# Performance work log

Hardware: AMD Instinct MI355X
Metric: run time of the kernel (lower is better)

## Reference

```python
import jax, jax.numpy as jnp
import numpy as np

N_NODES = 50000
N_EDGES = 800000
IN_FEATS = 128
HIDDEN = 256
N_CLASSES = 64


def setup_inputs() -> dict:
    key = jax.random.key(0)
    ks = jax.random.split(key, 16)
    def w(k, shape, fan_in):
        return jax.random.normal(k, shape, dtype=jnp.float32) * (1.0 / np.sqrt(fan_in))
    inp = {
        "x": jax.random.normal(ks[0], (N_NODES, IN_FEATS), dtype=jnp.float32),
        "edge_src": jax.random.randint(ks[1], (N_EDGES,), 0, N_NODES, dtype=jnp.int32),
        "edge_dst": jax.random.randint(ks[2], (N_EDGES,), 0, N_NODES, dtype=jnp.int32),
        # layer 0: in_feats -> hidden
        "W0s": w(ks[3], (IN_FEATS, HIDDEN), IN_FEATS),
        "W0n": w(ks[4], (IN_FEATS, HIDDEN), IN_FEATS),
        "b0": jnp.zeros((HIDDEN,), dtype=jnp.float32),
        # layer 1: hidden -> hidden
        "W1s": w(ks[5], (HIDDEN, HIDDEN), HIDDEN),
        "W1n": w(ks[6], (HIDDEN, HIDDEN), HIDDEN),
        "b1": jnp.zeros((HIDDEN,), dtype=jnp.float32),
        # layer 2: hidden -> hidden (last conv also outputs hidden per source code)
        "W2s": w(ks[7], (HIDDEN, HIDDEN), HIDDEN),
        "W2n": w(ks[8], (HIDDEN, HIDDEN), HIDDEN),
        "b2": jnp.zeros((HIDDEN,), dtype=jnp.float32),
        # fc1: hidden -> n_classes
        "Wfc": w(ks[9], (HIDDEN, N_CLASSES), HIDDEN),
        "bfc": jnp.zeros((N_CLASSES,), dtype=jnp.float32),
    }
    return inp


def _sage_layer(h, src, dst, Ws, Wn, b):
    # mean-neighbor aggregation: segment-sum messages, divide by in-degree
    msg = h[src]  # [E, D] irregular gather
    agg = jax.ops.segment_sum(msg, dst, num_segments=N_NODES)  # [N, D]
    deg = jax.ops.segment_sum(jnp.ones_like(dst, dtype=h.dtype), dst, num_segments=N_NODES)
    h_neigh = agg / jnp.maximum(deg, 1.0)[:, None]
    # DGL SAGEConv (mean): fc_self(h) + fc_neigh(h_neigh) + bias
    return h @ Ws + h_neigh @ Wn + b


def reference(x, edge_src, edge_dst, W0s, W0n, b0, W1s, W1n, b1, W2s, W2n, b2, Wfc, bfc):
    # forward applies dropout (identity at eval) and NO activation between layers,
    # matching the original module's forward().
    h = _sage_layer(x, edge_src, edge_dst, W0s, W0n, b0)
    h = _sage_layer(h, edge_src, edge_dst, W1s, W1n, b1)
    h = _sage_layer(h, edge_src, edge_dst, W2s, W2n, b2)
    return h @ Wfc + bfc  # [N, n_classes]
```

## Files before the change

kernel.cpp:

```cpp
#include <hip/hip_runtime.h>

#define NN 50000
#define NE 800000
#define NE_HALF 400000
#define F_IN 128
#define HID 256
#define N_CLS 64
#define SCAN_BLOCKS ((NN + 255) / 256)
#define HEPT 2
#define HBF ((NE + 256 * HEPT - 1) / (256 * HEPT))
#define HBH ((NE_HALF + 256 * HEPT - 1) / (256 * HEPT))
#define CF_BLOCKS 36
#define CL_BLOCKS 9
#define GA_BLOCKS ((NN + 127) / 128)
#define GG_BLOCKS ((NN + 31) / 32)
#define CROWS 515

typedef _Float16 half8 __attribute__((ext_vector_type(8)));
typedef float f32x4 __attribute__((ext_vector_type(4)));

__device__ __forceinline__ const float* virtC1_row(int r, const float* W0s,
                                                   const float* W0n, const float* b0) {
    if (r < 0) return nullptr;
    if (r < 128) return W0s + (size_t)r * 256;
    if (r < 256) return W0n + (size_t)(r - 128) * 256;
    if (r == 512) return b0;
    return nullptr;
}

__device__ __forceinline__ int shift_src(int r) {
    if (r >= 128 && r < 512) return r - 128;
    if (r == 513) return 512;
    if (r == 514) return 513;
    return -1;
}

__device__ __forceinline__ void compose_first_dev(
    int bx, const float* __restrict__ W0s, const float* __restrict__ W0n,
    const float* __restrict__ b0,
    const float* __restrict__ B1, const float* __restrict__ B2,
    const float* __restrict__ brow, float* __restrict__ C)
{
    __shared__ float As[64][17];
    __shared__ float Bs[16][64];
    const int tid = threadIdx.x;
    const int tx = tid & 15, ty = tid >> 4;
    const int row0 = (bx % 9) * 64;
    const int col0 = (bx / 9) * 64;
    const int lr = tid >> 2, lc = tid & 3;
    const int br = tid >> 4, bc = tid & 15;

    const int grow = row0 + lr;
    const int srcr0 = (grow < CROWS) ? grow : -1;
    const float* ap0 = virtC1_row(srcr0, W0s, W0n, b0);
    const float* ap1 = virtC1_row(shift_src(grow), W0s, W0n, b0);

    float acc[4][4] = {};

    float4 av = ap0 ? *(const float4*)(ap0 + lc * 4) : make_float4(0.f, 0.f, 0.f, 0.f);
    float4 bv = *(const float4*)(B1 + (size_t)br * 256 + col0 + bc * 4);

    for (int s = 0; s < 32; ++s) {
        As[lr][lc * 4 + 0] = av.x;
        As[lr][lc * 4 + 1] = av.y;
        As[lr][lc * 4 + 2] = av.z;
        As[lr][lc * 4 + 3] = av.w;
        *(float4*)&Bs[br][bc * 4] = bv;
        __syncthreads();
        if (s + 1 < 32) {
            int pass = (s + 1) >> 4;
            int k0 = ((s + 1) & 15) << 4;
            const float* ap = pass ? ap1 : ap0;
            const float* B = pass ? B2 : B1;
            av = ap ? *(const float4*)(ap + k0 + lc * 4) : make_float4(0.f, 0.f, 0.f, 0.f);
            bv = *(const float4*)(B + (size_t)(k0 + br) * 256 + col0 + bc * 4);
        }
        #pragma unroll
        for (int k = 0; k < 16; ++k) {
            float a[4];
            #pragma unroll
            for (int i = 0; i < 4; ++i) a[i] = As[ty * 4 + i][k];
            float4 bb = *(const float4*)&Bs[k][tx * 4];
            const float b[4] = {bb.x, bb.y, bb.z, bb.w};
            #pragma unroll
            for (int i = 0; i < 4; ++i)
                #pragma unroll
                for (int j = 0; j < 4; ++j)
                    acc[i][j] += a[i] * b[j];
        }
        __syncthreads();
    }

    #pragma unroll
    for (int i = 0; i < 4; ++i) {
        int r = row0 + ty * 4 + i;
        if (r < CROWS) {
            #pragma unroll
            for (int j = 0; j < 4; ++j) {
                float v = acc[i][j];
                if (r == 512) v += brow[col0 + tx * 4 + j];
                C[(size_t)r * 256 + col0 + tx * 4 + j] = v;
            }
        }
    }
}

__device__ __forceinline__ void compose_mid_dev(
    int bx, const float* __restrict__ A,
    const float* __restrict__ B1, const float* __restrict__ B2,
    const float* __restrict__ brow, float* __restrict__ C)
{
    __shared__ float As[64][17];
    __shared__ float Bs[16][64];
    const int tid = threadIdx.x;
    const int tx = tid & 15, ty = tid >> 4;
    const int row0 = (bx % 9) * 64;
    const int col0 = (bx / 9) * 64;
    const int lr = tid >> 2, lc = tid & 3;
    const int br = tid >> 4, bc = tid & 15;

    const int grow = row0 + lr;
    const int p0 = (grow < CROWS) ? grow : -1;
    const int p1 = shift_src(grow);

    float acc[4][4] = {};

    float4 av = (p0 >= 0) ? *(const float4*)(A + (size_t)p0 * 256 + lc * 4)
                          : make_float4(0.f, 0.f, 0.f, 0.f);
    float4 bv = *(const float4*)(B1 + (size_t)br * 256 + col0 + bc * 4);

    for (int s = 0; s < 32; ++s) {
        As[lr][lc * 4 + 0] = av.x;
        As[lr][lc * 4 + 1] = av.y;
        As[lr][lc * 4 + 2] = av.z;
        As[lr][lc * 4 + 3] = av.w;
        *(float4*)&Bs[br][bc * 4] = bv;
        __syncthreads();
        if (s + 1 < 32) {
            int pass = (s + 1) >> 4;
            int k0 = ((s + 1) & 15) << 4;
            int p = pass ? p1 : p0;
            const float* B = pass ? B2 : B1;
            av = (p >= 0) ? *(const float4*)(A + (size_t)p * 256 + k0 + lc * 4)
                          : make_float4(0.f, 0.f, 0.f, 0.f);
            bv = *(const float4*)(B + (size_t)(k0 + br) * 256 + col0 + bc * 4);
        }
        #pragma unroll
        for (int k = 0; k < 16; ++k) {
            float a[4];
            #pragma unroll
            for (int i = 0; i < 4; ++i) a[i] = As[ty * 4 + i][k];
            float4 bb = *(const float4*)&Bs[k][tx * 4];
            const float b[4] = {bb.x, bb.y, bb.z, bb.w};
            #pragma unroll
            for (int i = 0; i < 4; ++i)
                #pragma unroll
                for (int j = 0; j < 4; ++j)
                    acc[i][j] += a[i] * b[j];
        }
        __syncthreads();
    }

    #pragma unroll
    for (int i = 0; i < 4; ++i) {
        int r = row0 + ty * 4 + i;
        if (r < CROWS) {
            #pragma unroll
            for (int j = 0; j < 4; ++j) {
                float v = acc[i][j];
                if (r == 512) v += brow[col0 + tx * 4 + j];
                C[(size_t)r * 256 + col0 + tx * 4 + j] = v;
            }
        }
    }
}

__device__ __forceinline__ void compose_last_dev(
    int bx, const float* __restrict__ A, const float* __restrict__ B1,
    const float* __restrict__ brow, float* __restrict__ Vf, _Float16* __restrict__ BT)
{
    __shared__ float As[64][17];
    __shared__ float Bs[16][64];
    const int tid = threadIdx.x;
    const int tx = tid & 15, ty = tid >> 4;
    const int row0 = bx * 64;
    const int lr = tid >> 2, lc = tid & 3;
    const int br = tid >> 4, bc = tid & 15;

    const int grow = row0 + lr;
    const float* ap = (grow < CROWS) ? (A + (size_t)grow * 256) : nullptr;

    float acc[4][4] = {};

    float4 av = ap ? *(const float4*)(ap + lc * 4) : make_float4(0.f, 0.f, 0.f, 0.f);
    float4 bv = *(const float4*)(B1 + (size_t)br * 64 + bc * 4);

    for (int s = 0; s < 16; ++s) {
        As[lr][lc * 4 + 0] = av.x;
        As[lr][lc * 4 + 1] = av.y;
        As[lr][lc * 4 + 2] = av.z;
        As[lr][lc * 4 + 3] = av.w;
        *(float4*)&Bs[br][bc * 4] = bv;
        __syncthreads();
        if (s + 1 < 16) {
            int k0 = (s + 1) << 4;
            av = ap ? *(const float4*)(ap + k0 + lc * 4) : make_float4(0.f, 0.f, 0.f, 0.f);
            bv = *(const float4*)(B1 + (size_t)(k0 + br) * 64 + bc * 4);
        }
        #pragma unroll
        for (int k = 0; k < 16; ++k) {
            float a[4];
            #pragma unroll
            for (int i = 0; i < 4; ++i) a[i] = As[ty * 4 + i][k];
            float4 bb = *(const float4*)&Bs[k][tx * 4];
            const float b[4] = {bb.x, bb.y, bb.z, bb.w};
            #pragma unroll
            for (int i = 0; i < 4; ++i)
                #pragma unroll
                for (int j = 0; j < 4; ++j)
                    acc[i][j] += a[i] * b[j];
        }
        __syncthreads();
    }

    #pragma unroll
    for (int i = 0; i < 4; ++i) {
        int r = row0 + ty * 4 + i;
        if (r < CROWS) {
            #pragma unroll
            for (int j = 0; j < 4; ++j) {
                int c = tx * 4 + j;
                float v = acc[i][j];
                if (r == 512) v += brow[c];
                Vf[(size_t)r * 64 + c] = v;
                if (r < 512)
                    BT[(size_t)((r >> 7) * 64 + c) * 128 + (r & 127)] = (_Float16)v;
            }
        }
    }
}

__device__ __forceinline__ void hist_dev(int bx, int start, int count,
                                         const int* __restrict__ edst,
                                         int* __restrict__ cnt,
                                         unsigned short* __restrict__ rank) {
    int base = start + bx * (256 * HEPT) + threadIdx.x;
    int lim = start + count;
    int d[HEPT];
    #pragma unroll
    for (int k = 0; k < HEPT; ++k) {
        int e = base + k * 256;
        d[k] = (e < lim) ? edst[e] : -1;
    }
    #pragma unroll
    for (int k = 0; k < HEPT; ++k) {
        int e = base + k * 256;
        if (d[k] >= 0) rank[e] = (unsigned short)atomicAdd(&cnt[d[k]], 1);
    }
}

__device__ __forceinline__ void scan_full_dev(const int* __restrict__ cnt,
                                              int* __restrict__ offs,
                                              float* __restrict__ dinv, int bx) {
    __shared__ int s[256];
    const int t = threadIdx.x;
    const int limit = bx * 256;
    int p = 0;
    for (int i = t; i < limit; i += 256) p += cnt[i];
    s[t] = p;
    __syncthreads();
    for (int off = 128; off > 0; off >>= 1) {
        if (t < off) s[t] += s[t + off];
        __syncthreads();
    }
    const int base = s[0];
    __syncthreads();
    int i = limit + t;
    int v = (i < NN) ? cnt[i] : 0;
    s[t] = v;
    __syncthreads();
    for (int off = 1; off < 256; off <<= 1) {
        int u = (t >= off) ? s[t - off] : 0;
        __syncthreads();
        s[t] += u;
        __syncthreads();
    }
    if (i < NN) {
        offs[i] = base + s[t] - v;
        dinv[i] = 1.0f / (float)max(v, 1);
    }
    if (i == NN - 1) offs[NN] = base + s[t];
}

__device__ __forceinline__ void gemm_y_dev(
    int bx, int by,
    const float* __restrict__ X, const _Float16* __restrict__ BT,
    _Float16* __restrict__ Y, _Float16* __restrict__ Tc, int N)
{
    constexpr int LP = 40;
    __shared__ _Float16 As[128 * LP];
    __shared__ _Float16 Bs[128 * LP];

    const int tid = threadIdx.x;
    const int wave = tid >> 6;
    const int lane = tid & 63;
    const int l15 = lane & 15;
    const int quad = lane >> 4;
    const int wrow = wave >> 1;
    const int wcol = wave & 1;
    const int m_base = wrow * 64;
    const int n_base = wcol * 64;

    const int row0 = bx * 128;
    const int col0 = by * 128;

    f32x4 acc[4][4] = {};

    for (int k0 = 0; k0 < 128; k0 += 32) {
        #pragma unroll
        for (int r = 0; r < 2; ++r) {
            int idx = r * 256 + tid;
            int row = idx >> 2, ch = idx & 3;
            int gr = row0 + row; if (gr > N - 1) gr = N - 1;
            const float* ap = X + (size_t)gr * 128 + k0 + ch * 8;
            float4 f0 = *(const float4*)ap;
            float4 f1 = *(const float4*)(ap + 4);
            half8 v = { (_Float16)f0.x, (_Float16)f0.y, (_Float16)f0.z, (_Float16)f0.w,
                        (_Float16)f1.x, (_Float16)f1.y, (_Float16)f1.z, (_Float16)f1.w };
            *(half8*)&As[row * LP + ch * 8] = v;
        }
        #pragma unroll
        for (int r = 0; r < 2; ++r) {
            int idx = r * 256 + tid;
            int row = idx >> 2, ch = idx & 3;
            *(half8*)&Bs[row * LP + ch * 8] =
                *(const half8*)(BT + (size_t)(col0 + row) * 128 + k0 + ch * 8);
        }
        __syncthreads();
        half8 af[4], bf[4];
        #pragma unroll
        for (int i = 0; i < 4; ++i)
            af[i] = *(const half8*)&As[(m_base + i * 16 + l15) * LP + quad * 8];
        #pragma unroll
        for (int j = 0; j < 4; ++j)
            bf[j] = *(const half8*)&Bs[(n_base + j * 16 + l15) * LP + quad * 8];
        #pragma unroll
        for (int i = 0; i < 4; ++i)
            #pragma unroll
            for (int j = 0; j < 4; ++j)
                acc[i][j] = __builtin_amdgcn_mfma_f32_16x16x32_f16(af[i], bf[j], acc[i][j], 0, 0, 0);
        __syncthreads();
    }

    #pragma unroll
    for (int i = 0; i < 4; ++i) {
        #pragma unroll
        for (int j = 0; j < 4; ++j) {
            int col = col0 + n_base + j * 16 + l15;
            #pragma unroll
            for (int r = 0; r < 4; ++r) {
                int row = row0 + m_base + i * 16 + quad * 4 + r;
                if (row < N) {
                    _Float16 v = (_Float16)acc[i][j][r];
                    Y[(size_t)row * 256 + col] = v;
                    if (col >= 192) Tc[(size_t)row * 64 + (col - 192)] = v;
                }
            }
        }
    }
}

template <bool OUT_F32>
__device__ __forceinline__ void gather_node_dev(
    int node, int lane,
    const _Float16* __restrict__ Tin,
    const unsigned short* __restrict__ csr, const int* __restrict__ offs,
    const float* __restrict__ dinv,
    const _Float16* __restrict__ Yadd,
    const float* __restrict__ cvec,
    void* __restrict__ Tout)
{
    int beg = offs[node], end = offs[node + 1];
    float acc[8] = {};
    int e = beg;
    for (; e + 7 < end; e += 8) {
        int s0 = csr[e], s1 = csr[e + 1], s2 = csr[e + 2], s3 = csr[e + 3];
        int s4 = csr[e + 4], s5 = csr[e + 5], s6 = csr[e + 6], s7 = csr[e + 7];
        half8 v0 = *(const half8*)(Tin + (size_t)s0 * 64 + lane * 8);
        half8 v1 = *(const half8*)(Tin + (size_t)s1 * 64 + lane * 8);
        half8 v2 = *(const half8*)(Tin + (size_t)s2 * 64 + lane * 8);
        half8 v3 = *(const half8*)(Tin + (size_t)s3 * 64 + lane * 8);
        half8 v4 = *(const half8*)(Tin + (size_t)s4 * 64 + lane * 8);
        half8 v5 = *(const half8*)(Tin + (size_t)s5 * 64 + lane * 8);
        half8 v6 = *(const half8*)(Tin + (size_t)s6 * 64 + lane * 8);
        half8 v7 = *(const half8*)(Tin + (size_t)s7 * 64 + lane * 8);
        #pragma unroll
        for (int j = 0; j < 8; ++j)
            acc[j] += (((float)v0[j] + (float)v1[j]) + ((float)v2[j] + (float)v3[j]))
                    + (((float)v4[j] + (float)v5[j]) + ((float)v6[j] + (float)v7[j]));
    }
    for (; e + 3 < end; e += 4) {
        int s0 = csr[e], s1 = csr[e + 1], s2 = csr[e + 2], s3 = csr[e + 3];
        half8 v0 = *(const half8*)(Tin + (size_t)s0 * 64 + lane * 8);
        half8 v1 = *(const half8*)(Tin + (size_t)s1 * 64 + lane * 8);
        half8 v2 = *(const half8*)(Tin + (size_t)s2 * 64 + lane * 8);
        half8 v3 = *(const half8*)(Tin + (size_t)s3 * 64 + lane * 8);
        #pragma unroll
        for (int j = 0; j < 8; ++j)
            acc[j] += ((float)v0[j] + (float)v1[j]) + ((float)v2[j] + (float)v3[j]);
    }
    for (; e < end; ++e) {
        half8 v = *(const half8*)(Tin + (size_t)csr[e] * 64 + lane * 8);
        #pragma unroll
        for (int j = 0; j < 8; ++j) acc[j] += (float)v[j];
    }
    float sc = dinv[node];
    half8 y = *(const half8*)(Yadd + (size_t)node * 256 + lane * 8);
    if (OUT_F32) {
        float* o = (float*)Tout + (size_t)node * 64 + lane * 8;
        float4 o0, o1;
        o0.x = acc[0] * sc + (float)y[0] + cvec[lane * 8 + 0];
        o0.y = acc[1] * sc + (float)y[1] + cvec[lane * 8 + 1];
        o0.z = acc[2] * sc + (float)y[2] + cvec[lane * 8 + 2];
        o0.w = acc[3] * sc + (float)y[3] + cvec[lane * 8 + 3];
        o1.x = acc[4] * sc + (float)y[4] + cvec[lane * 8 + 4];
        o1.y = acc[5] * sc + (float)y[5] + cvec[lane * 8 + 5];
        o1.z = acc[6] * sc + (float)y[6] + cvec[lane * 8 + 6];
        o1.w = acc[7] * sc + (float)y[7] + cvec[lane * 8 + 7];
        *(float4*)o = o0;
        *(float4*)(o + 4) = o1;
    } else {
        half8 o;
        #pragma unroll
        for (int j = 0; j < 8; ++j)
            o[j] = (_Float16)(acc[j] * sc + (float)y[j] + cvec[lane * 8 + j]);
        *(half8*)((_Float16*)Tout + (size_t)node * 64 + lane * 8) = o;
    }
}

__global__ __launch_bounds__(256) void k_composeF_hist(
    const int* __restrict__ edst, int* __restrict__ cnt, unsigned short* __restrict__ rank,
    const float* __restrict__ W0s, const float* __restrict__ W0n, const float* __restrict__ b0,
    const float* __restrict__ W1s, const float* __restrict__ W1n, const float* __restrict__ b1,
    float* __restrict__ C2)
{
    if (blockIdx.x < CF_BLOCKS) {
        compose_first_dev(blockIdx.x, W0s, W0n, b0, W1s, W1n, b1, C2);
    } else {
        hist_dev(blockIdx.x - CF_BLOCKS, 0, NE_HALF, edst, cnt, rank);
    }
}

__global__ __launch_bounds__(256) void k_composeM_hist2(
    const int* __restrict__ edst, int* __restrict__ cnt, unsigned short* __restrict__ rank,
    const float* __restrict__ C2,
    const float* __restrict__ W2s, const float* __restrict__ W2n, const float* __restrict__ b2,
    float* __restrict__ C3)
{
    if (blockIdx.x < CF_BLOCKS) compose_mid_dev(blockIdx.x, C2, W2s, W2n, b2, C3);
    else hist_dev(blockIdx.x - CF_BLOCKS, NE_HALF, NE - NE_HALF, edst, cnt, rank);
}

__global__ __launch_bounds__(256) void k_composeL_scan(
    const int* __restrict__ cnt, int* __restrict__ offs, float* __restrict__ dinv,
    const float* __restrict__ C3, const float* __restrict__ Wfc, const float* __restrict__ bfc,
    float* __restrict__ Vf, _Float16* __restrict__ BT)
{
    if (blockIdx.x < CL_BLOCKS) compose_last_dev(blockIdx.x, C3, Wfc, bfc, Vf, BT);
    else scan_full_dev(cnt, offs, dinv, blockIdx.x - CL_BLOCKS);
}

__global__ __launch_bounds__(256) void k_gemmT_place(
    const int* __restrict__ esrc, const int* __restrict__ edst,
    const unsigned short* __restrict__ rank, const int* __restrict__ offs,
    unsigned short* __restrict__ csr,
    const float* __restrict__ X, const _Float16* __restrict__ BT,
    _Float16* __restrict__ Y, _Float16* __restrict__ Tc)
{
    if (blockIdx.x < GA_BLOCKS) {
        gemm_y_dev(blockIdx.x, 1, X, BT, Y, Tc, NN);
    } else {
        int base = (blockIdx.x - GA_BLOCKS) * (256 * HEPT) + threadIdx.x;
        int d[HEPT], s[HEPT], r[HEPT];
        #pragma unroll
        for (int k = 0; k < HEPT; ++k) {
            int e = base + k * 256;
            if (e < NE) { d[k] = edst[e]; s[k] = esrc[e]; r[k] = rank[e]; }
            else d[k] = -1;
        }
        #pragma unroll
        for (int k = 0; k < HEPT; ++k) {
            if (d[k] >= 0) csr[offs[d[k]] + r[k]] = (unsigned short)s[k];
        }
    }
}

__global__ __launch_bounds__(256) void k_gemmA_gather1(
    const float* __restrict__ X, const _Float16* __restrict__ BT,
    _Float16* __restrict__ Y, _Float16* __restrict__ Tc,
    const unsigned short* __restrict__ csr, const int* __restrict__ offs,
    const float* __restrict__ dinv, const float* __restrict__ Vf,
    _Float16* __restrict__ Ta)
{
    if (blockIdx.x < GA_BLOCKS) {
        gemm_y_dev(blockIdx.x, 0, X, BT, Y, Tc, NN);
    } else {
        int node = (blockIdx.x - GA_BLOCKS) * 32 + (threadIdx.x >> 3);
        int lane = threadIdx.x & 7;
        if (node < NN)
            gather_node_dev<false>(node, lane, Tc, csr, offs, dinv,
                                   Y + 128, Vf + (size_t)514 * 64, (void*)Ta);
    }
}

template <bool OUT_F32>
__global__ __launch_bounds__(256) void gather64(
    const _Float16* __restrict__ Tin,
    const unsigned short* __restrict__ csr, const int* __restrict__ offs,
    const float* __restrict__ dinv,
    const _Float16* __restrict__ Yadd,
    const float* __restrict__ cvec,
    void* __restrict__ Tout, int N)
{
    int node = blockIdx.x * 32 + (threadIdx.x >> 3);
    int lane = threadIdx.x & 7;
    if (node >= N) return;
    gather_node_dev<OUT_F32>(node, lane, Tin, csr, offs, dinv, Yadd, cvec, Tout);
}

extern "C" void kernel_launch(void* const* d_in, const int* in_sizes, int n_in,
                              void* d_out, int out_size, void* d_ws, size_t ws_size,
                              hipStream_t stream) {
    const float* x    = (const float*)d_in[0];
    const int*   esrc = (const int*)d_in[1];
    const int*   edst = (const int*)d_in[2];
    const float* W0s  = (const float*)d_in[3];
    const float* W0n  = (const float*)d_in[4];
    const float* b0   = (const float*)d_in[5];
    const float* W1s  = (const float*)d_in[6];
    const float* W1n  = (const float*)d_in[7];
    const float* b1   = (const float*)d_in[8];
    const float* W2s  = (const float*)d_in[9];
    const float* W2n  = (const float*)d_in[10];
    const float* b2   = (const float*)d_in[11];
    const float* Wfc  = (const float*)d_in[12];
    const float* bfc  = (const float*)d_in[13];
    float* out = (float*)d_out;

    _Float16* Y   = (_Float16*)d_ws;
    _Float16* Ta  = Y + (size_t)NN * 256;
    _Float16* Tb  = Ta + (size_t)NN * 64;
    _Float16* Tc  = Tb + (size_t)NN * 64;
    _Float16* BT  = Tc + (size_t)NN * 64;
    float* C2     = (float*)(BT + 256 * 128);
    float* C3     = C2 + CROWS * 256;
    float* Vf     = C3 + CROWS * 256;
    float* dinv   = Vf + CROWS * 64;
    int* cnt      = (int*)(dinv + NN);
    int* offs     = cnt + NN;
    int* blockSums = offs + NN + 1;
    unsigned short* rank = (unsigned short*)(blockSums + SCAN_BLOCKS);
    unsigned short* csr  = rank + NE;

    hipMemsetAsync(cnt, 0, (size_t)NN * sizeof(int), stream);

    k_composeF_hist<<<CF_BLOCKS + HBH, 256, 0, stream>>>(
        edst, cnt, rank, W0s, W0n, b0, W1s, W1n, b1, C2);

    k_composeM_hist2<<<CF_BLOCKS + HBH, 256, 0, stream>>>(
        edst, cnt, rank, C2, W2s, W2n, b2, C3);

    k_composeL_scan<<<CL_BLOCKS + SCAN_BLOCKS, 256, 0, stream>>>(
        cnt, offs, dinv, C3, Wfc, bfc, Vf, BT);

    k_gemmT_place<<<GA_BLOCKS + HBF, 256, 0, stream>>>(
        esrc, edst, rank, offs, csr, x, BT, Y, Tc);

    k_gemmA_gather1<<<GA_BLOCKS + GG_BLOCKS, 256, 0, stream>>>(
        x, BT, Y, Tc, csr, offs, dinv, Vf, Ta);

    gather64<false><<<GG_BLOCKS, 256, 0, stream>>>(
        Ta, csr, offs, dinv, Y + 64, Vf + (size_t)513 * 64, (void*)Tb, NN);
    gather64<true><<<GG_BLOCKS, 256, 0, stream>>>(
        Tb, csr, offs, dinv, Y, Vf + (size_t)512 * 64, (void*)out, NN);
}
```

Measured before the change: 284.4 us.

## Reassociate weight composition and merge launches into fewer fused kernels

The weight-chain composition is reassociated: W2s·Wfc and W2n·Wfc (plus the combined bias) are precomputed in parallel with the first composition and the edge histogram. The separate mid and last compose stages become a single 515x64 compose. This removes one full 515x256x512 GEMM stage and one kernel launch. The whole histogram now runs in one kernel with 4 edges per thread. Both node GEMM passes run together with CSR placement. The first gather becomes its own launch, so it no longer overlaps with a GEMM.

```diff
diff --git a/kernel.cpp b/kernel.cpp
--- a/kernel.cpp
+++ b/kernel.cpp
@@ -2,16 +2,15 @@
 
 #define NN 50000
 #define NE 800000
-#define NE_HALF 400000
 #define F_IN 128
 #define HID 256
 #define N_CLS 64
 #define SCAN_BLOCKS ((NN + 255) / 256)
-#define HEPT 2
+#define HEPT 4
 #define HBF ((NE + 256 * HEPT - 1) / (256 * HEPT))
-#define HBH ((NE_HALF + 256 * HEPT - 1) / (256 * HEPT))
 #define CF_BLOCKS 36
-#define CL_BLOCKS 9
+#define PRE_BLOCKS 9
+#define CFIN_BLOCKS 9
 #define GA_BLOCKS ((NN + 127) / 128)
 #define GG_BLOCKS ((NN + 31) / 32)
 #define CROWS 515
@@ -105,45 +104,44 @@
     }
 }
 
-__device__ __forceinline__ void compose_mid_dev(
-    int bx, const float* __restrict__ A,
-    const float* __restrict__ B1, const float* __restrict__ B2,
-    const float* __restrict__ brow, float* __restrict__ C)
-{
+__device__ __forceinline__ void precompute_dev(
+    int p, const float* __restrict__ W2s, const float* __restrict__ W2n,
+    const float* __restrict__ b2, const float* __restrict__ Wfc, const float* __restrict__ bfc,
+    float* __restrict__ Wcs, float* __restrict__ Wcn, float* __restrict__ bcv)
+{
+    const int tid = threadIdx.x;
+    if (p == 8) {
+        if (tid < 64) {
+            float s = bfc[tid];
+            for (int k = 0; k < 256; ++k) s += b2[k] * Wfc[(size_t)k * 64 + tid];
+            bcv[tid] = s;
+        }
+        return;
+    }
     __shared__ float As[64][17];
     __shared__ float Bs[16][64];
-    const int tid = threadIdx.x;
     const int tx = tid & 15, ty = tid >> 4;
-    const int row0 = (bx % 9) * 64;
-    const int col0 = (bx / 9) * 64;
     const int lr = tid >> 2, lc = tid & 3;
     const int br = tid >> 4, bc = tid & 15;
-
-    const int grow = row0 + lr;
-    const int p0 = (grow < CROWS) ? grow : -1;
-    const int p1 = shift_src(grow);
+    const float* M = (p < 4) ? W2s : W2n;
+    float* O = (p < 4) ? Wcs : Wcn;
+    const int row0 = (p & 3) * 64;
 
     float acc[4][4] = {};
-
-    float4 av = (p0 >= 0) ? *(const float4*)(A + (size_t)p0 * 256 + lc * 4)
-                          : make_float4(0.f, 0.f, 0.f, 0.f);
-    float4 bv = *(const float4*)(B1 + (size_t)br * 256 + col0 + bc * 4);
-
-    for (int s = 0; s < 32; ++s) {
+    float4 av = *(const float4*)(M + (size_t)(row0 + lr) * 256 + lc * 4);
+    float4 bv = *(const float4*)(Wfc + (size_t)br * 64 + bc * 4);
+
+    for (int s = 0; s < 16; ++s) {
         As[lr][lc * 4 + 0] = av.x;
         As[lr][lc * 4 + 1] = av.y;
         As[lr][lc * 4 + 2] = av.z;
         As[lr][lc * 4 + 3] = av.w;
         *(float4*)&Bs[br][bc * 4] = bv;
         __syncthreads();
-        if (s + 1 < 32) {
-            int pass = (s + 1) >> 4;
-            int k0 = ((s + 1) & 15) << 4;
-            int p = pass ? p1 : p0;
-            const float* B = pass ? B2 : B1;
-            av = (p >= 0) ? *(const float4*)(A + (size_t)p * 256 + k0 + lc * 4)
-                          : make_float4(0.f, 0.f, 0.f, 0.f);
-            bv = *(const float4*)(B + (size_t)(k0 + br) * 256 + col0 + bc * 4);
+        if (s + 1 < 16) {
+            int k0 = (s + 1) << 4;
+            av = *(const float4*)(M + (size_t)(row0 + lr) * 256 + k0 + lc * 4);
+            bv = *(const float4*)(Wfc + (size_t)(k0 + br) * 64 + bc * 4);
         }
         #pragma unroll
         for (int k = 0; k < 16; ++k) {
@@ -160,24 +158,18 @@
         }
         __syncthreads();
     }
-
     #pragma unroll
-    for (int i = 0; i < 4; ++i) {
-        int r = row0 + ty * 4 + i;
-        if (r < CROWS) {
-            #pragma unroll
-            for (int j = 0; j < 4; ++j) {
-                float v = acc[i][j];
-                if (r == 512) v += brow[col0 + tx * 4 + j];
-                C[(size_t)r * 256 + col0 + tx * 4 + j] = v;
-            }
-        }
-    }
-}
-
-__device__ __forceinline__ void compose_last_dev(
-    int bx, const float* __restrict__ A, const float* __restrict__ B1,
-    const float* __restrict__ brow, float* __restrict__ Vf, _Float16* __restrict__ BT)
+    for (int i = 0; i < 4; ++i)
+        #pragma unroll
+        for (int j = 0; j < 4; ++j)
+            O[(size_t)(row0 + ty * 4 + i) * 64 + tx * 4 + j] = acc[i][j];
+}
+
+__device__ __forceinline__ void compose_fin_dev(
+    int bx, const float* __restrict__ C2,
+    const float* __restrict__ Wcs, const float* __restrict__ Wcn,
+    const float* __restrict__ bcv,
+    float* __restrict__ Vf, _Float16* __restrict__ BT)
 {
     __shared__ float As[64][17];
     __shared__ float Bs[16][64];
@@ -188,24 +180,30 @@
     const int br = tid >> 4, bc = tid & 15;
 
     const int grow = row0 + lr;
-    const float* ap = (grow < CROWS) ? (A + (size_t)grow * 256) : nullptr;
+    const int p0 = (grow < CROWS) ? grow : -1;
+    const int p1 = shift_src(grow);
 
     float acc[4][4] = {};
 
-    float4 av = ap ? *(const float4*)(ap + lc * 4) : make_float4(0.f, 0.f, 0.f, 0.f);
-    float4 bv = *(const float4*)(B1 + (size_t)br * 64 + bc * 4);
-
-    for (int s = 0; s < 16; ++s) {
+    float4 av = (p0 >= 0) ? *(const float4*)(C2 + (size_t)p0 * 256 + lc * 4)
+                          : make_float4(0.f, 0.f, 0.f, 0.f);
+    float4 bv = *(const float4*)(Wcs + (size_t)br * 64 + bc * 4);
+
+    for (int s = 0; s < 32; ++s) {
         As[lr][lc * 4 + 0] = av.x;
         As[lr][lc * 4 + 1] = av.y;
         As[lr][lc * 4 + 2] = av.z;
         As[lr][lc * 4 + 3] = av.w;
         *(float4*)&Bs[br][bc * 4] = bv;
         __syncthreads();
-        if (s + 1 < 16) {
-            int k0 = (s + 1) << 4;
-            av = ap ? *(const float4*)(ap + k0 + lc * 4) : make_float4(0.f, 0.f, 0.f, 0.f);
-            bv = *(const float4*)(B1 + (size_t)(k0 + br) * 64 + bc * 4);
+        if (s + 1 < 32) {
+            int pass = (s + 1) >> 4;
+            int k0 = ((s + 1) & 15) << 4;
+            int p = pass ? p1 : p0;
+            const float* B = pass ? Wcn : Wcs;
+            av = (p >= 0) ? *(const float4*)(C2 + (size_t)p * 256 + k0 + lc * 4)
+                          : make_float4(0.f, 0.f, 0.f, 0.f);
+            bv = *(const float4*)(B + (size_t)(k0 + br) * 64 + bc * 4);
         }
         #pragma unroll
         for (int k = 0; k < 16; ++k) {
@@ -231,7 +229,7 @@
             for (int j = 0; j < 4; ++j) {
                 int c = tx * 4 + j;
                 float v = acc[i][j];
-                if (r == 512) v += brow[c];
+                if (r == 512) v += bcv[c];
                 Vf[(size_t)r * 64 + c] = v;
                 if (r < 512)
                     BT[(size_t)((r >> 7) * 64 + c) * 128 + (r & 127)] = (_Float16)v;
@@ -240,17 +238,15 @@
     }
 }
 
-__device__ __forceinline__ void hist_dev(int bx, int start, int count,
-                                         const int* __restrict__ edst,
+__device__ __forceinline__ void hist_dev(int bx, const int* __restrict__ edst,
                                          int* __restrict__ cnt,
                                          unsigned short* __restrict__ rank) {
-    int base = start + bx * (256 * HEPT) + threadIdx.x;
-    int lim = start + count;
+    int base = bx * (256 * HEPT) + threadIdx.x;
     int d[HEPT];
     #pragma unroll
     for (int k = 0; k < HEPT; ++k) {
         int e = base + k * 256;
-        d[k] = (e < lim) ? edst[e] : -1;
+        d[k] = (e < NE) ? edst[e] : -1;
     }
     #pragma unroll
     for (int k = 0; k < HEPT; ++k) {
@@ -438,39 +434,35 @@
     }
 }
 
-__global__ __launch_bounds__(256) void k_composeF_hist(
+__global__ __launch_bounds__(256) void k_CF_pre_hist(
     const int* __restrict__ edst, int* __restrict__ cnt, unsigned short* __restrict__ rank,
     const float* __restrict__ W0s, const float* __restrict__ W0n, const float* __restrict__ b0,
     const float* __restrict__ W1s, const float* __restrict__ W1n, const float* __restrict__ b1,
-    float* __restrict__ C2)
+    const float* __restrict__ W2s, const float* __restrict__ W2n, const float* __restrict__ b2,
+    const float* __restrict__ Wfc, const float* __restrict__ bfc,
+    float* __restrict__ C2, float* __restrict__ Wcs, float* __restrict__ Wcn,
+    float* __restrict__ bcv)
 {
     if (blockIdx.x < CF_BLOCKS) {
         compose_first_dev(blockIdx.x, W0s, W0n, b0, W1s, W1n, b1, C2);
+    } else if (blockIdx.x < CF_BLOCKS + PRE_BLOCKS) {
+        precompute_dev(blockIdx.x - CF_BLOCKS, W2s, W2n, b2, Wfc, bfc, Wcs, Wcn, bcv);
     } else {
-        hist_dev(blockIdx.x - CF_BLOCKS, 0, NE_HALF, edst, cnt, rank);
-    }
-}
-
-__global__ __launch_bounds__(256) void k_composeM_hist2(
-    const int* __restrict__ edst, int* __restrict__ cnt, unsigned short* __restrict__ rank,
-    const float* __restrict__ C2,
-    const float* __restrict__ W2s, const float* __restrict__ W2n, const float* __restrict__ b2,
-    float* __restrict__ C3)
-{
-    if (blockIdx.x < CF_BLOCKS) compose_mid_dev(blockIdx.x, C2, W2s, W2n, b2, C3);
-    else hist_dev(blockIdx.x - CF_BLOCKS, NE_HALF, NE - NE_HALF, edst, cnt, rank);
-}
-
-__global__ __launch_bounds__(256) void k_composeL_scan(
+        hist_dev(blockIdx.x - CF_BLOCKS - PRE_BLOCKS, edst, cnt, rank);
+    }
+}
+
+__global__ __launch_bounds__(256) void k_CFin_scan(
     const int* __restrict__ cnt, int* __restrict__ offs, float* __restrict__ dinv,
-    const float* __restrict__ C3, const float* __restrict__ Wfc, const float* __restrict__ bfc,
+    const float* __restrict__ C2, const float* __restrict__ Wcs,
+    const float* __restrict__ Wcn, const float* __restrict__ bcv,
     float* __restrict__ Vf, _Float16* __restrict__ BT)
 {
-    if (blockIdx.x < CL_BLOCKS) compose_last_dev(blockIdx.x, C3, Wfc, bfc, Vf, BT);
-    else scan_full_dev(cnt, offs, dinv, blockIdx.x - CL_BLOCKS);
-}
-
-__global__ __launch_bounds__(256) void k_gemmT_place(
+    if (blockIdx.x < CFIN_BLOCKS) compose_fin_dev(blockIdx.x, C2, Wcs, Wcn, bcv, Vf, BT);
+    else scan_full_dev(cnt, offs, dinv, blockIdx.x - CFIN_BLOCKS);
+}
+
+__global__ __launch_bounds__(256) void k_gemm_place(
     const int* __restrict__ esrc, const int* __restrict__ edst,
     const unsigned short* __restrict__ rank, const int* __restrict__ offs,
     unsigned short* __restrict__ csr,
@@ -479,8 +471,10 @@
 {
     if (blockIdx.x < GA_BLOCKS) {
         gemm_y_dev(blockIdx.x, 1, X, BT, Y, Tc, NN);
+    } else if (blockIdx.x < 2 * GA_BLOCKS) {
+        gemm_y_dev(blockIdx.x - GA_BLOCKS, 0, X, BT, Y, Tc, NN);
     } else {
-        int base = (blockIdx.x - GA_BLOCKS) * (256 * HEPT) + threadIdx.x;
+        int base = (blockIdx.x - 2 * GA_BLOCKS) * (256 * HEPT) + threadIdx.x;
         int d[HEPT], s[HEPT], r[HEPT];
         #pragma unroll
         for (int k = 0; k < HEPT; ++k) {
@@ -492,24 +486,6 @@
         for (int k = 0; k < HEPT; ++k) {
             if (d[k] >= 0) csr[offs[d[k]] + r[k]] = (unsigned short)s[k];
         }
-    }
-}
-
-__global__ __launch_bounds__(256) void k_gemmA_gather1(
-    const float* __restrict__ X, const _Float16* __restrict__ BT,
-    _Float16* __restrict__ Y, _Float16* __restrict__ Tc,
-    const unsigned short* __restrict__ csr, const int* __restrict__ offs,
-    const float* __restrict__ dinv, const float* __restrict__ Vf,
-    _Float16* __restrict__ Ta)
-{
-    if (blockIdx.x < GA_BLOCKS) {
-        gemm_y_dev(blockIdx.x, 0, X, BT, Y, Tc, NN);
-    } else {
-        int node = (blockIdx.x - GA_BLOCKS) * 32 + (threadIdx.x >> 3);
-        int lane = threadIdx.x & 7;
-        if (node < NN)
-            gather_node_dev<false>(node, lane, Tc, csr, offs, dinv,
-                                   Y + 128, Vf + (size_t)514 * 64, (void*)Ta);
     }
 }
 
@@ -553,32 +529,30 @@
     _Float16* Tc  = Tb + (size_t)NN * 64;
     _Float16* BT  = Tc + (size_t)NN * 64;
     float* C2     = (float*)(BT + 256 * 128);
-    float* C3     = C2 + CROWS * 256;
-    float* Vf     = C3 + CROWS * 256;
+    float* Wcs    = C2 + CROWS * 256;
+    float* Wcn    = Wcs + 256 * 64;
+    float* bcv    = Wcn + 256 * 64;
+    float* Vf     = bcv + 64;
     float* dinv   = Vf + CROWS * 64;
     int* cnt      = (int*)(dinv + NN);
     int* offs     = cnt + NN;
-    int* blockSums = offs + NN + 1;
-    unsigned short* rank = (unsigned short*)(blockSums + SCAN_BLOCKS);
+    unsigned short* rank = (unsigned short*)(offs + NN + 1);
     unsigned short* csr  = rank + NE;
 
     hipMemsetAsync(cnt, 0, (size_t)NN * sizeof(int), stream);
 
-    k_composeF_hist<<<CF_BLOCKS + HBH, 256, 0, stream>>>(
-        edst, cnt, rank, W0s, W0n, b0, W1s, W1n, b1, C2);
-
-    k_composeM_hist2<<<CF_BLOCKS + HBH, 256, 0, stream>>>(
-        edst, cnt, rank, C2, W2s, W2n, b2, C3);
-
-    k_composeL_scan<<<CL_BLOCKS + SCAN_BLOCKS, 256, 0, stream>>>(
-        cnt, offs, dinv, C3, Wfc, bfc, Vf, BT);
-
-    k_gemmT_place<<<GA_BLOCKS + HBF, 256, 0, stream>>>(
+    k_CF_pre_hist<<<CF_BLOCKS + PRE_BLOCKS + HBF, 256, 0, stream>>>(
+        edst, cnt, rank, W0s, W0n, b0, W1s, W1n, b1,
+        W2s, W2n, b2, Wfc, bfc, C2, Wcs, Wcn, bcv);
+
+    k_CFin_scan<<<CFIN_BLOCKS + SCAN_BLOCKS, 256, 0, stream>>>(
+        cnt, offs, dinv, C2, Wcs, Wcn, bcv, Vf, BT);
+
+    k_gemm_place<<<2 * GA_BLOCKS + HBF, 256, 0, stream>>>(
         esrc, edst, rank, offs, csr, x, BT, Y, Tc);
 
-    k_gemmA_gather1<<<GA_BLOCKS + GG_BLOCKS, 256, 0, stream>>>(
-        x, BT, Y, Tc, csr, offs, dinv, Vf, Ta);
-
+    gather64<false><<<GG_BLOCKS, 256, 0, stream>>>(
+        Tc, csr, offs, dinv, Y + 128, Vf + (size_t)514 * 64, (void*)Ta, NN);
     gather64<false><<<GG_BLOCKS, 256, 0, stream>>>(
         Ta, csr, offs, dinv, Y + 64, Vf + (size_t)513 * 64, (void*)Tb, NN);
     gather64<true><<<GG_BLOCKS, 256, 0, stream>>>(
```

Result: faster. 252.9 us (-11.1%).
